# Kernel tuning notes

Measured on AMD Instinct MI355X. Metric: run time of the kernel, lower is better.

The kernel has to match this reference:

```python
import jax, jax.numpy as jnp
import numpy as np

N_NODES = 50000
N_EDGES = 800000
F_IN = 128
HEADS = 4
C_OUT = 32
NEG_SLOPE = 0.2
BN_EPS = 1e-5


def _add_self_loops(edge_index, edge_attr, n):
    # PyG fill_value='mean': self-loop attr = mean of incoming edge attrs per node (0 if none)
    src, dst = edge_index[0], edge_index[1]
    deg = jax.ops.segment_sum(jnp.ones_like(edge_attr[:, 0]), dst, num_segments=n)
    loop_attr = jax.ops.segment_sum(edge_attr, dst, num_segments=n) / jnp.maximum(deg, 1.0)[:, None]
    loop = jnp.arange(n)
    src2 = jnp.concatenate([src, loop])
    dst2 = jnp.concatenate([dst, loop])
    attr2 = jnp.concatenate([edge_attr, loop_attr], axis=0)
    return src2, dst2, attr2


def _segment_softmax(logits, seg, n):
    m = jax.ops.segment_max(logits, seg, num_segments=n)
    m = jnp.where(jnp.isfinite(m), m, 0.0)
    ex = jnp.exp(logits - m[seg])
    s = jax.ops.segment_sum(ex, seg, num_segments=n)
    return ex / s[seg]


def _gatv2(x, src, dst, eattr, Wl, bl, Wr, br, We, att, bias, n):
    # x: [n, F]; returns [n, HEADS*C_OUT]
    xl = (x @ Wl + bl).reshape(n, HEADS, C_OUT)
    xr = (x @ Wr + br).reshape(n, HEADS, C_OUT)
    ea = (eattr @ We).reshape(-1, HEADS, C_OUT)
    xlj = xl[src]                                   # [E, H, C] gather
    msg = jax.nn.leaky_relu(xlj + xr[dst] + ea, NEG_SLOPE)
    logits = jnp.einsum('ehc,hc->eh', msg, att)     # [E, H]
    alpha = _segment_softmax(logits, dst, n)
    out = jax.ops.segment_sum(xlj * alpha[..., None], dst, num_segments=n)
    return out.reshape(n, HEADS * C_OUT) + bias


def _batchnorm(x, gamma, beta):
    mu = x.mean(axis=0)
    var = x.var(axis=0)
    return gamma * (x - mu) * jax.lax.rsqrt(var + BN_EPS) + beta


def setup_inputs() -> dict:
    key = jax.random.key(0)
    ks = jax.random.split(key, 20)
    HC = HEADS * C_OUT
    s = 0.05
    inp = {
        'emb': jax.random.normal(ks[0], (N_NODES, F_IN), dtype=jnp.float32),
        'edge_index': jax.random.randint(ks[1], (2, N_EDGES), 0, N_NODES, dtype=jnp.int64),
        'edge_weight': jax.random.uniform(ks[2], (N_EDGES, 1), dtype=jnp.float32),
        'Wl1': jax.random.normal(ks[3], (F_IN, HC)) * s,
        'bl1': jnp.zeros((HC,), jnp.float32),
        'Wr1': jax.random.normal(ks[4], (F_IN, HC)) * s,
        'br1': jnp.zeros((HC,), jnp.float32),
        'We1': jax.random.normal(ks[5], (1, HC)) * s,
        'att1': jax.random.normal(ks[6], (HEADS, C_OUT)) * s,
        'bias1': jnp.zeros((HC,), jnp.float32),
        'gamma1': jnp.ones((HC,), jnp.float32),
        'beta1': jnp.zeros((HC,), jnp.float32),
        'Wl2': jax.random.normal(ks[7], (HC, HC)) * s,
        'bl2': jnp.zeros((HC,), jnp.float32),
        'Wr2': jax.random.normal(ks[8], (HC, HC)) * s,
        'br2': jnp.zeros((HC,), jnp.float32),
        'We2': jax.random.normal(ks[9], (1, HC)) * s,
        'att2': jax.random.normal(ks[10], (HEADS, C_OUT)) * s,
        'bias2': jnp.zeros((HC,), jnp.float32),
    }
    return inp


def reference(emb, edge_index, edge_weight, Wl1, bl1, Wr1, br1, We1, att1, bias1,
              gamma1, beta1, Wl2, bl2, Wr2, br2, We2, att2, bias2):
    n = emb.shape[0]
    src, dst, eattr = _add_self_loops(edge_index, edge_weight, n)
    h1 = _gatv2(emb, src, dst, eattr, Wl1, bl1, Wr1, br1, We1, att1, bias1, n)
    h1 = jax.nn.elu(_batchnorm(h1, gamma1, beta1))
    h2 = _gatv2(h1, src, dst, eattr, Wl2, bl2, Wr2, br2, We2, att2, bias2, n)
    # fusion: mean over [input_emb, h1, h2] along stacked axis
    return (emb + h1 + h2) / 3.0
```

## Files before the change

### kernel.cpp

```cpp
#include <hip/hip_runtime.h>
#include <hip/hip_bf16.h>
#include <math.h>

#define N_NODES 50000
#define N_EDGES 800000
#define HC 128
#define SLOT 64

#define BM 128
#define NBX ((N_NODES + BM - 1) / BM)
#define NB_EDGE ((N_EDGES + 255) / 256)

typedef short bh8 __attribute__((ext_vector_type(8)));
typedef float f4 __attribute__((ext_vector_type(4)));
typedef float f2 __attribute__((ext_vector_type(2)));

__device__ __forceinline__ unsigned int pk2(float a, float b) {
  return (unsigned int)__bfloat16_as_ushort(__float2bfloat16(a)) |
         ((unsigned int)__bfloat16_as_ushort(__float2bfloat16(b)) << 16);
}

__global__ __launch_bounds__(256) void k_wprep(
    const float* __restrict__ Wl1, const float* __restrict__ Wr1,
    const float* __restrict__ Wl2, const float* __restrict__ Wr2,
    unsigned short* __restrict__ WtAll, int* __restrict__ cursor,
    float* __restrict__ chsum, float* __restrict__ chsq) {
  int gid = blockIdx.x * 256 + threadIdx.x;
  int m = gid >> 14;
  int idx = gid & 16383;
  const float* src = (m == 0) ? Wl1 : (m == 1) ? Wr1 : (m == 2) ? Wl2 : Wr2;
  int k = idx >> 7, n = idx & 127;
  WtAll[((size_t)m * HC + n) * HC + k] =
      __bfloat16_as_ushort(__float2bfloat16(src[k * HC + n]));
  if (gid < N_NODES) cursor[gid] = 0;
  if (gid < HC) { chsum[gid] = 0.f; chsq[gid] = 0.f; }
}

template <int LAYER2, int F8>
__device__ __forceinline__ void gemm_tile(
    int bx, const float* __restrict__ X, const unsigned short* __restrict__ Wt,
    const float* __restrict__ b0, const float* __restrict__ b1,
    void* __restrict__ Y0, float* __restrict__ Y1,
    const float* __restrict__ chsum, const float* __restrict__ chsq,
    const float* __restrict__ gamma, const float* __restrict__ beta) {
  __shared__ __align__(16) unsigned short Xls[128 * 128];
  __shared__ __align__(16) unsigned short Wls[128 * 128];
  __shared__ float ssc[HC], ssh[HC];
  int tid = threadIdx.x;
  if (LAYER2) {
    if (tid < HC) {
      float mu = chsum[tid] * (1.f / N_NODES);
      float var = chsq[tid] * (1.f / N_NODES) - mu * mu;
      float sc = gamma[tid] * rsqrtf(var + 1e-5f);
      ssc[tid] = sc;
      ssh[tid] = beta[tid] - mu * sc;
    }
    __syncthreads();
  }
  int row0 = bx * BM;
  {
    int r = tid >> 1;
    int ks = (tid & 1) * 64;
    int gr = row0 + r;
    const float* xp = X + (size_t)gr * HC + ks;
    int sw = r & 15;
#pragma unroll
    for (int i = 0; i < 4; ++i) {
      float f[16];
      if (gr < N_NODES) {
        *(float4*)&f[0] = *(const float4*)(xp + i * 16);
        *(float4*)&f[4] = *(const float4*)(xp + i * 16 + 4);
        *(float4*)&f[8] = *(const float4*)(xp + i * 16 + 8);
        *(float4*)&f[12] = *(const float4*)(xp + i * 16 + 12);
      } else {
#pragma unroll
        for (int j = 0; j < 16; ++j) f[j] = 0.f;
      }
      if (LAYER2) {
#pragma unroll
        for (int j = 0; j < 16; ++j) {
          float y = fmaf(f[j], ssc[ks + i * 16 + j], ssh[ks + i * 16 + j]);
          f[j] = (y > 0.f) ? y : (__expf(y) - 1.f);
        }
      }
      int kg = (ks >> 3) + i * 2;
      *(uint4*)&Xls[r * 128 + ((kg ^ sw) * 8)] =
          make_uint4(pk2(f[0], f[1]), pk2(f[2], f[3]), pk2(f[4], f[5]), pk2(f[6], f[7]));
      *(uint4*)&Xls[r * 128 + (((kg + 1) ^ sw) * 8)] =
          make_uint4(pk2(f[8], f[9]), pk2(f[10], f[11]), pk2(f[12], f[13]), pk2(f[14], f[15]));
    }
  }
  int lane = tid & 63;
  int wv = tid >> 6;
  int lrow = lane & 15;
  int lq = lane >> 4;
  int rbase = wv * 32;
#pragma unroll
  for (int half = 0; half < 2; ++half) {
    if (half) __syncthreads();
    {
      int n = tid >> 1;
      int ks = (tid & 1) * 64;
      const unsigned short* wp = Wt + half * (HC * HC) + n * HC + ks;
      int swn = n & 15;
#pragma unroll
      for (int g = 0; g < 8; ++g) {
        uint4 v = *(const uint4*)(wp + g * 8);
        int kg = (ks >> 3) + g;
        *(uint4*)&Wls[n * 128 + ((kg ^ swn) * 8)] = v;
      }
    }
    __syncthreads();
    f4 acc[2][8];
#pragma unroll
    for (int mt = 0; mt < 2; ++mt)
#pragma unroll
      for (int nt = 0; nt < 8; ++nt) acc[mt][nt] = (f4){0.f, 0.f, 0.f, 0.f};
#pragma unroll
    for (int kk = 0; kk < 4; ++kk) {
      int kg = kk * 4 + lq;
      bh8 a0 = *(const bh8*)&Xls[(rbase + lrow) * 128 + ((kg ^ lrow) * 8)];
      bh8 a1 = *(const bh8*)&Xls[(rbase + 16 + lrow) * 128 + ((kg ^ lrow) * 8)];
#pragma unroll
      for (int nt = 0; nt < 8; ++nt) {
        bh8 b = *(const bh8*)&Wls[(nt * 16 + lrow) * 128 + ((kg ^ lrow) * 8)];
        acc[0][nt] = __builtin_amdgcn_mfma_f32_16x16x32_bf16(a0, b, acc[0][nt], 0, 0, 0);
        acc[1][nt] = __builtin_amdgcn_mfma_f32_16x16x32_bf16(a1, b, acc[1][nt], 0, 0, 0);
      }
    }
    const float* bb = half ? b1 : b0;
    float bv[8];
#pragma unroll
    for (int nt = 0; nt < 8; ++nt) bv[nt] = bb[nt * 16 + lrow];
#pragma unroll
    for (int mt = 0; mt < 2; ++mt) {
#pragma unroll
      for (int rr = 0; rr < 4; ++rr) {
        int gr = row0 + rbase + mt * 16 + lq * 4 + rr;
        if (gr < N_NODES) {
          if (half == 0) {
            if (F8) {
#pragma unroll
              for (int nt = 0; nt < 8; ++nt) {
                float v = acc[mt][nt][rr] + bv[nt];
                int p = __builtin_amdgcn_cvt_pk_fp8_f32(v, v, 0, false);
                ((unsigned char*)Y0)[(size_t)gr * HC + nt * 16 + lrow] =
                    (unsigned char)(p & 0xff);
              }
            } else {
#pragma unroll
              for (int nt = 0; nt < 8; ++nt)
                ((unsigned short*)Y0)[(size_t)gr * HC + nt * 16 + lrow] =
                    __bfloat16_as_ushort(__float2bfloat16(acc[mt][nt][rr] + bv[nt]));
            }
          } else {
#pragma unroll
            for (int nt = 0; nt < 8; ++nt)
              Y1[(size_t)gr * HC + nt * 16 + lrow] = acc[mt][nt][rr] + bv[nt];
          }
        }
      }
    }
  }
}

__global__ __launch_bounds__(256) void k_g1prep(
    const float* __restrict__ X, const unsigned short* __restrict__ Wt,
    const float* __restrict__ b0, const float* __restrict__ b1,
    unsigned short* __restrict__ Y0b, float* __restrict__ Y1,
    const int* __restrict__ ei, const float* __restrict__ ew,
    int* __restrict__ cursor, unsigned int* __restrict__ slots) {
  int bid = blockIdx.x;
  if (bid < NBX) {
    gemm_tile<0, 0>(bid, X, Wt, b0, b1, (void*)Y0b, Y1, nullptr, nullptr,
                    nullptr, nullptr);
    return;
  }
  int e = (bid - NBX) * 256 + threadIdx.x;
  if (e >= N_EDGES) return;
  int s = ei[e];
  int d = ei[N_EDGES + e];
  float w = ew[e];
  unsigned int wq = min((unsigned int)(w * 65536.f + 0.5f), 65535u);
  int pos = atomicAdd(cursor + d, 1);
  if (pos < SLOT) {
    slots[(size_t)d * SLOT + pos] = ((unsigned int)s << 16) | wq;
  }
}

__global__ __launch_bounds__(256) void k_gemm2(
    const float* __restrict__ X, const unsigned short* __restrict__ Wt,
    const float* __restrict__ b0, const float* __restrict__ b1,
    unsigned char* __restrict__ Y0f8, float* __restrict__ Y1,
    const float* __restrict__ chsum, const float* __restrict__ chsq,
    const float* __restrict__ gamma, const float* __restrict__ beta) {
  gemm_tile<1, 1>(blockIdx.x, X, Wt, b0, b1, (void*)Y0f8, Y1, chsum, chsq,
                  gamma, beta);
}

template <int FINAL, int F8>
__global__ __launch_bounds__(256) void k_gat(
    const void* __restrict__ xlv, const float* __restrict__ xr,
    const int* __restrict__ cursor, const unsigned int* __restrict__ slots,
    const float* __restrict__ We, const float* __restrict__ att,
    const float* __restrict__ bias, float* __restrict__ out,
    const float* __restrict__ emb, const float* __restrict__ h1p,
    const float* __restrict__ chsum, const float* __restrict__ chsq,
    const float* __restrict__ gamma, const float* __restrict__ beta) {
  int g = threadIdx.x >> 5;
  int lane = threadIdx.x & 31;
  int n = blockIdx.x * 8 + g;
  int fi = n * 32 + lane;
  const uint2* xl2 = (const uint2*)xlv;
  const unsigned int* xf = (const unsigned int*)xlv;
  float4 xr4 = ((const float4*)xr)[fi];
  float4 we4 = ((const float4*)We)[lane];
  float4 at4 = ((const float4*)att)[lane];
  int deg = min(cursor[n], SLOT);
  int base = n * SLOT;
  int deg32 = min(deg, 32);

  unsigned int ev = (lane < deg32) ? slots[base + lane] : 0u;
  float evw = (float)(ev & 0xffffu) * (1.f / 65536.f);
  float wsum = evw;
#pragma unroll
  for (int m = 16; m >= 1; m >>= 1) wsum += __shfl_xor(wsum, m);

  float l = 0.f;
  float4 o = make_float4(0.f, 0.f, 0.f, 0.f);

  auto decode = [&](uint2 gc) -> float4 {
    float4 xlj;
    if (F8) {
      f2 ab = __builtin_amdgcn_cvt_pk_f32_fp8((int)gc.x, false);
      f2 cd = __builtin_amdgcn_cvt_pk_f32_fp8((int)gc.x, true);
      xlj.x = ab[0]; xlj.y = ab[1]; xlj.z = cd[0]; xlj.w = cd[1];
    } else {
      xlj.x = __uint_as_float(gc.x << 16);
      xlj.y = __uint_as_float(gc.x & 0xffff0000u);
      xlj.z = __uint_as_float(gc.y << 16);
      xlj.w = __uint_as_float(gc.y & 0xffff0000u);
    }
    return xlj;
  };
  auto edge_body = [&](float w, uint2 gc, bool valid) {
    float4 xlj = decode(gc);
    float4 v;
    v.x = fmaf(w, we4.x, xlj.x + xr4.x);
    v.y = fmaf(w, we4.y, xlj.y + xr4.y);
    v.z = fmaf(w, we4.z, xlj.z + xr4.z);
    v.w = fmaf(w, we4.w, xlj.w + xr4.w);
    v.x = fmaxf(v.x, 0.2f * v.x);
    v.y = fmaxf(v.y, 0.2f * v.y);
    v.z = fmaxf(v.z, 0.2f * v.z);
    v.w = fmaxf(v.w, 0.2f * v.w);
    float p = v.x * at4.x + v.y * at4.y + v.z * at4.z + v.w * at4.w;
    p += __shfl_xor(p, 1);
    p += __shfl_xor(p, 2);
    p += __shfl_xor(p, 4);
    float e = valid ? __expf(p) : 0.f;
    l += e;
    o.x = fmaf(e, xlj.x, o.x);
    o.y = fmaf(e, xlj.y, o.y);
    o.z = fmaf(e, xlj.z, o.z);
    o.w = fmaf(e, xlj.w, o.w);
  };
  auto fetch = [&](int j, uint2& qq, float& ww) {
    int jc = min(j, deg32 - 1);
    unsigned int evj = __shfl(ev, jc, 32);
    ww = (float)(evj & 0xffffu) * (1.f / 65536.f);
    int s = (int)(evj >> 16);
    if (F8) qq.x = xf[s * 32 + lane];
    else qq = xl2[s * 32 + lane];
  };

  if (deg32 > 0) {
    uint2 q0, q1, q2, q3;
    float w0, w1, w2, w3;
    fetch(0, q0, w0);
    fetch(1, q1, w1);
    fetch(2, q2, w2);
    fetch(3, q3, w3);
    for (int b = 0; b < deg32; b += 4) {
      uint2 c0 = q0, c1 = q1, c2 = q2, c3 = q3;
      float x0 = w0, x1 = w1, x2 = w2, x3 = w3;
      fetch(b + 4, q0, w0);
      fetch(b + 5, q1, w1);
      fetch(b + 6, q2, w2);
      fetch(b + 7, q3, w3);
      edge_body(x0, c0, true);
      edge_body(x1, c1, b + 1 < deg32);
      edge_body(x2, c2, b + 2 < deg32);
      edge_body(x3, c3, b + 3 < deg32);
    }
  }
  if (deg > 32) {
    for (int j = base + 32; j < base + deg; ++j) {
      unsigned int evj = slots[j];
      float w = (float)(evj & 0xffffu) * (1.f / 65536.f);
      wsum += w;
      int s = (int)(evj >> 16);
      uint2 gc;
      if (F8) gc.x = xf[s * 32 + lane];
      else gc = xl2[s * 32 + lane];
      edge_body(w, gc, true);
    }
  }
  {
    float wself = (deg > 0) ? wsum / (float)deg : 0.f;
    uint2 gs;
    if (F8) gs.x = xf[n * 32 + lane];
    else gs = xl2[n * 32 + lane];
    edge_body(wself, gs, true);
  }

  float inv = 1.f / l;
  float4 b4 = ((const float4*)bias)[lane];
  float4 r;
  r.x = fmaf(o.x, inv, b4.x);
  r.y = fmaf(o.y, inv, b4.y);
  r.z = fmaf(o.z, inv, b4.z);
  r.w = fmaf(o.w, inv, b4.w);
  if (FINAL) {
    float4 e4 = ((const float4*)emb)[fi];
    float4 h4 = ((const float4*)h1p)[fi];
    float4 cs = ((const float4*)chsum)[lane];
    float4 cq = ((const float4*)chsq)[lane];
    float4 gm = ((const float4*)gamma)[lane];
    float4 bt = ((const float4*)beta)[lane];
    const float invN = 1.f / N_NODES;
    float4 sc4, sh4;
    {
      float mu = cs.x * invN, var = cq.x * invN - mu * mu;
      sc4.x = gm.x * rsqrtf(var + 1e-5f); sh4.x = bt.x - mu * sc4.x;
      mu = cs.y * invN; var = cq.y * invN - mu * mu;
      sc4.y = gm.y * rsqrtf(var + 1e-5f); sh4.y = bt.y - mu * sc4.y;
      mu = cs.z * invN; var = cq.z * invN - mu * mu;
      sc4.z = gm.z * rsqrtf(var + 1e-5f); sh4.z = bt.z - mu * sc4.z;
      mu = cs.w * invN; var = cq.w * invN - mu * mu;
      sc4.w = gm.w * rsqrtf(var + 1e-5f); sh4.w = bt.w - mu * sc4.w;
    }
    float4 h;
    h.x = fmaf(h4.x, sc4.x, sh4.x);
    h.y = fmaf(h4.y, sc4.y, sh4.y);
    h.z = fmaf(h4.z, sc4.z, sh4.z);
    h.w = fmaf(h4.w, sc4.w, sh4.w);
    h.x = (h.x > 0.f) ? h.x : (__expf(h.x) - 1.f);
    h.y = (h.y > 0.f) ? h.y : (__expf(h.y) - 1.f);
    h.z = (h.z > 0.f) ? h.z : (__expf(h.z) - 1.f);
    h.w = (h.w > 0.f) ? h.w : (__expf(h.w) - 1.f);
    const float k3 = 1.f / 3.f;
    r.x = (e4.x + h.x + r.x) * k3;
    r.y = (e4.y + h.y + r.y) * k3;
    r.z = (e4.z + h.z + r.z) * k3;
    r.w = (e4.w + h.w + r.w) * k3;
  }
  ((float4*)out)[fi] = r;
}

#define BN_ROWS 200
__global__ __launch_bounds__(256) void k_bnstats(const float* __restrict__ h1,
                                                 float* __restrict__ chsum,
                                                 float* __restrict__ chsq) {
  int c = threadIdx.x & 127;
  int g = threadIdx.x >> 7;
  int r0 = blockIdx.x * BN_ROWS;
  float s = 0.f, q = 0.f;
  for (int r = r0 + g; r < r0 + BN_ROWS; r += 2) {
    float v = h1[(size_t)r * HC + c];
    s += v;
    q += v * v;
  }
  __shared__ float sh[256], shq[256];
  sh[threadIdx.x] = s;
  shq[threadIdx.x] = q;
  __syncthreads();
  if (g == 0) {
    atomicAdd(chsum + c, s + sh[threadIdx.x + 128]);
    atomicAdd(chsq + c, q + shq[threadIdx.x + 128]);
  }
}

extern "C" void kernel_launch(void* const* d_in, const int* in_sizes, int n_in,
                              void* d_out, int out_size, void* d_ws, size_t ws_size,
                              hipStream_t stream) {
  const float* emb = (const float*)d_in[0];
  const int* ei = (const int*)d_in[1];
  const float* ew = (const float*)d_in[2];
  const float* Wl1 = (const float*)d_in[3];
  const float* bl1 = (const float*)d_in[4];
  const float* Wr1 = (const float*)d_in[5];
  const float* br1 = (const float*)d_in[6];
  const float* We1 = (const float*)d_in[7];
  const float* att1 = (const float*)d_in[8];
  const float* bias1 = (const float*)d_in[9];
  const float* gamma1 = (const float*)d_in[10];
  const float* beta1 = (const float*)d_in[11];
  const float* Wl2 = (const float*)d_in[12];
  const float* bl2 = (const float*)d_in[13];
  const float* Wr2 = (const float*)d_in[14];
  const float* br2 = (const float*)d_in[15];
  const float* We2 = (const float*)d_in[16];
  const float* att2 = (const float*)d_in[17];
  const float* bias2 = (const float*)d_in[18];
  float* out = (float*)d_out;

  char* wsb = (char*)d_ws;
  size_t off = 0;
  auto alloc = [&](size_t bytes) -> void* {
    void* p = (void*)(wsb + off);
    off += (bytes + 255) & ~(size_t)255;
    return p;
  };
  int* cursor = (int*)alloc((size_t)N_NODES * 4);
  float* chsum = (float*)alloc(HC * 4);
  float* chsq = (float*)alloc(HC * 4);
  unsigned short* WtAll = (unsigned short*)alloc((size_t)4 * HC * HC * 2);
  unsigned int* slots = (unsigned int*)alloc((size_t)N_NODES * SLOT * 4);
  unsigned short* xlb = (unsigned short*)alloc((size_t)N_NODES * HC * 2);
  unsigned char* xlf8 = (unsigned char*)alloc((size_t)N_NODES * HC);
  float* xr = (float*)alloc((size_t)N_NODES * HC * 4);
  float* h1 = (float*)alloc((size_t)N_NODES * HC * 4);

  k_wprep<<<256, 256, 0, stream>>>(Wl1, Wr1, Wl2, Wr2, WtAll, cursor, chsum, chsq);
  k_g1prep<<<NBX + NB_EDGE, 256, 0, stream>>>(emb, WtAll, bl1, br1, xlb, xr,
                                              ei, ew, cursor, slots);
  k_gat<0, 0><<<N_NODES / 8, 256, 0, stream>>>(xlb, xr, cursor, slots, We1, att1,
                                               bias1, h1, nullptr, nullptr,
                                               nullptr, nullptr, nullptr, nullptr);
  k_bnstats<<<N_NODES / BN_ROWS, 256, 0, stream>>>(h1, chsum, chsq);
  k_gemm2<<<NBX, 256, 0, stream>>>(h1, WtAll + 2 * HC * HC, bl2, br2, xlf8, xr,
                                   chsum, chsq, gamma1, beta1);
  k_gat<1, 1><<<N_NODES / 8, 256, 0, stream>>>(xlf8, xr, cursor, slots, We2, att2,
                                               bias2, out, emb, h1, chsum, chsq,
                                               gamma1, beta1);
}
```

Baseline: 295.2 us.

## Read GEMM B-fragments from global memory and vectorize edge bucketing four per thread

```diff
diff --git a/kernel.cpp b/kernel.cpp
--- a/kernel.cpp
+++ b/kernel.cpp
@@ -9,7 +9,7 @@
 
 #define BM 128
 #define NBX ((N_NODES + BM - 1) / BM)
-#define NB_EDGE ((N_EDGES + 255) / 256)
+#define NB_EDGE ((N_EDGES / 4 + 255) / 256)
 
 typedef short bh8 __attribute__((ext_vector_type(8)));
 typedef float f4 __attribute__((ext_vector_type(4)));
@@ -44,7 +44,6 @@
     const float* __restrict__ chsum, const float* __restrict__ chsq,
     const float* __restrict__ gamma, const float* __restrict__ beta) {
   __shared__ __align__(16) unsigned short Xls[128 * 128];
-  __shared__ __align__(16) unsigned short Wls[128 * 128];
   __shared__ float ssc[HC], ssh[HC];
   int tid = threadIdx.x;
   if (LAYER2) {
@@ -90,27 +89,22 @@
           make_uint4(pk2(f[8], f[9]), pk2(f[10], f[11]), pk2(f[12], f[13]), pk2(f[14], f[15]));
     }
   }
+  __syncthreads();
   int lane = tid & 63;
   int wv = tid >> 6;
   int lrow = lane & 15;
   int lq = lane >> 4;
   int rbase = wv * 32;
+  bh8 afr[4][2];
+#pragma unroll
+  for (int kk = 0; kk < 4; ++kk) {
+    int kg = kk * 4 + lq;
+    afr[kk][0] = *(const bh8*)&Xls[(rbase + lrow) * 128 + ((kg ^ lrow) * 8)];
+    afr[kk][1] = *(const bh8*)&Xls[(rbase + 16 + lrow) * 128 + ((kg ^ lrow) * 8)];
+  }
 #pragma unroll
   for (int half = 0; half < 2; ++half) {
-    if (half) __syncthreads();
-    {
-      int n = tid >> 1;
-      int ks = (tid & 1) * 64;
-      const unsigned short* wp = Wt + half * (HC * HC) + n * HC + ks;
-      int swn = n & 15;
-#pragma unroll
-      for (int g = 0; g < 8; ++g) {
-        uint4 v = *(const uint4*)(wp + g * 8);
-        int kg = (ks >> 3) + g;
-        *(uint4*)&Wls[n * 128 + ((kg ^ swn) * 8)] = v;
-      }
-    }
-    __syncthreads();
+    const unsigned short* wbase = Wt + half * (HC * HC);
     f4 acc[2][8];
 #pragma unroll
     for (int mt = 0; mt < 2; ++mt)
@@ -119,11 +113,11 @@
 #pragma unroll
     for (int kk = 0; kk < 4; ++kk) {
       int kg = kk * 4 + lq;
-      bh8 a0 = *(const bh8*)&Xls[(rbase + lrow) * 128 + ((kg ^ lrow) * 8)];
-      bh8 a1 = *(const bh8*)&Xls[(rbase + 16 + lrow) * 128 + ((kg ^ lrow) * 8)];
+      bh8 a0 = afr[kk][0];
+      bh8 a1 = afr[kk][1];
 #pragma unroll
       for (int nt = 0; nt < 8; ++nt) {
-        bh8 b = *(const bh8*)&Wls[(nt * 16 + lrow) * 128 + ((kg ^ lrow) * 8)];
+        bh8 b = *(const bh8*)(wbase + (nt * 16 + lrow) * HC + kg * 8);
         acc[0][nt] = __builtin_amdgcn_mfma_f32_16x16x32_bf16(a0, b, acc[0][nt], 0, 0, 0);
         acc[1][nt] = __builtin_amdgcn_mfma_f32_16x16x32_bf16(a1, b, acc[1][nt], 0, 0, 0);
       }
@@ -176,15 +170,23 @@
                     nullptr, nullptr);
     return;
   }
-  int e = (bid - NBX) * 256 + threadIdx.x;
+  int e = ((bid - NBX) * 256 + threadIdx.x) * 4;
   if (e >= N_EDGES) return;
-  int s = ei[e];
-  int d = ei[N_EDGES + e];
-  float w = ew[e];
-  unsigned int wq = min((unsigned int)(w * 65536.f + 0.5f), 65535u);
-  int pos = atomicAdd(cursor + d, 1);
-  if (pos < SLOT) {
-    slots[(size_t)d * SLOT + pos] = ((unsigned int)s << 16) | wq;
+  int4 s4 = *(const int4*)(ei + e);
+  int4 d4 = *(const int4*)(ei + N_EDGES + e);
+  float4 w4 = *(const float4*)(ew + e);
+  int ss[4] = {s4.x, s4.y, s4.z, s4.w};
+  int dd[4] = {d4.x, d4.y, d4.z, d4.w};
+  float ww[4] = {w4.x, w4.y, w4.z, w4.w};
+  int pos[4];
+#pragma unroll
+  for (int i = 0; i < 4; ++i) pos[i] = atomicAdd(cursor + dd[i], 1);
+#pragma unroll
+  for (int i = 0; i < 4; ++i) {
+    unsigned int wq = min((unsigned int)(ww[i] * 65536.f + 0.5f), 65535u);
+    if (pos[i] < SLOT) {
+      slots[(size_t)dd[i] * SLOT + pos[i]] = ((unsigned int)ss[i] << 16) | wq;
+    }
   }
 }
 
```

After: 303.1 us. 1.03x slower.
